# Kernel optimization log

Hardware: AMD Instinct MI355X
Metric: run time of the kernel (lower is better)

The kernel has to match this reference:

```python
import jax, jax.numpy as jnp
import numpy as np

B, N, A, O, D, Q, H = 64, 4, 1024, 128, 256, 256, 128
NEG_INF = -1e30


def setup_inputs() -> dict:
    key = jax.random.key(0)
    ks = jax.random.split(key, 8)
    q = jax.random.normal(ks[0], (B, N, 1, Q), dtype=jnp.float32)
    att1 = jax.random.uniform(ks[1], (B, N, A, O), dtype=jnp.float32)
    obj_reps = jax.random.normal(ks[2], (B, O, D), dtype=jnp.float32)
    tags_attention = jax.random.randint(ks[3], (B, N, A), 0, 2, dtype=jnp.int32)
    W1 = jax.random.normal(ks[4], (D + Q, H), dtype=jnp.float32) / np.sqrt(D + Q)
    b1 = jnp.zeros((H,), dtype=jnp.float32)
    W2 = jax.random.normal(ks[5], (H, 1), dtype=jnp.float32) / np.sqrt(H)
    b2 = jnp.zeros((1,), dtype=jnp.float32)
    return {"q": q, "att1": att1, "obj_reps": obj_reps,
            "tags_attention": tags_attention,
            "W1": W1, "b1": b1, "W2": W2, "b2": b2, "t": 1}


def reference(q, att1, obj_reps, tags_attention, W1, b1, W2, b2, t):
    # v: [B,N,A,D] = att1 [B,N,A,O] @ obj_reps [B,O,D]
    v = jnp.einsum('bnao,bod->bnad', att1, obj_reps)
    # q broadcast over token dim A, concat -> [B,N,A,D+Q]
    q_proj = jnp.broadcast_to(q, v.shape[:3] + (q.shape[-1],))
    vq = jnp.concatenate([v, q_proj], axis=-1)
    # FCNet: Linear + ReLU (dropout is identity at inference)
    joint_repr = jax.nn.relu(vq @ W1 + b1)          # [B,N,A,H]
    logits = (joint_repr @ W2 + b2)[..., 0]          # [B,N,A]
    # temperature-scaled masked softmax over tokens
    masked = jnp.where(tags_attention > 0, logits / t, NEG_INF)
    att2 = jax.nn.softmax(masked, axis=-1)           # [B,N,A]
    # attention_last: [B,N,O] = att2 [B,N,1,A] @ att1 [B,N,A,O]
    return jnp.einsum('bna,bnao->bno', att2, att1)
```

## Files before the change

kernel.cpp:

```cpp
#include <hip/hip_runtime.h>
#include <math.h>

#define Bc 64
#define Nc 4
#define Ac 1024
#define Oc 128
#define Dc 256
#define Qc 256
#define Hc 128
#define BN (Bc*Nc)

using f4     = __attribute__((ext_vector_type(4))) float;
using f32x16 = __attribute__((ext_vector_type(16))) float;
using short8 = __attribute__((ext_vector_type(8))) short;
using us4    = __attribute__((ext_vector_type(4))) unsigned short;

__device__ inline float decode_t(const void* p) {
    int i = *(const int*)p;
    if (i >= 1 && i <= 1000000) return (float)i;
    return __int_as_float(i);
}

__device__ inline unsigned short bf16_rne(float x) {
    unsigned u = __builtin_bit_cast(unsigned, x);
    u += 0x7FFFu + ((u >> 16) & 1u);
    return (unsigned short)(u >> 16);
}

__device__ inline void split_bf16(float x, unsigned short& hi, unsigned short& lo) {
    unsigned u = __builtin_bit_cast(unsigned, x);
    hi = (unsigned short)(u >> 16);
    float hif = __builtin_bit_cast(float, u & 0xFFFF0000u);
    float lof = x - hif;
    lo = (unsigned short)(__builtin_bit_cast(unsigned, lof) >> 16);
}

__global__ __launch_bounds__(256) void prep_M_kernel(
    const float* __restrict__ obj, const float* __restrict__ W1,
    unsigned short* __restrict__ Mt_hi, unsigned short* __restrict__ Mt_lo)
{
    __shared__ float w_s[32][36];
    __shared__ float obj_sT[32][68];

    const int t  = threadIdx.x;
    const int tx = t & 15;
    const int ty = t >> 4;
    const int h0 = blockIdx.x * 32;
    const int o0 = blockIdx.y * 64;
    const int b  = blockIdx.z;
    const int r8 = t >> 3, c8 = t & 7;

    const float* objb = obj + ((size_t)b * Oc + o0) * Dc;

    float acc[2][4];
    #pragma unroll
    for (int i = 0; i < 2; i++)
        #pragma unroll
        for (int j = 0; j < 4; j++) acc[i][j] = 0.f;

    f4 wv  = *(const f4*)(W1 + (size_t)r8 * Hc + h0 + c8 * 4);
    f4 ov0 = *(const f4*)(objb + (size_t)r8 * Dc + c8 * 4);
    f4 ov1 = *(const f4*)(objb + (size_t)(r8 + 32) * Dc + c8 * 4);

    for (int ko = 0; ko < 8; ++ko) {
        *(f4*)&w_s[r8][c8 * 4] = wv;
        obj_sT[c8 * 4 + 0][r8] = ov0[0];
        obj_sT[c8 * 4 + 1][r8] = ov0[1];
        obj_sT[c8 * 4 + 2][r8] = ov0[2];
        obj_sT[c8 * 4 + 3][r8] = ov0[3];
        obj_sT[c8 * 4 + 0][r8 + 32] = ov1[0];
        obj_sT[c8 * 4 + 1][r8 + 32] = ov1[1];
        obj_sT[c8 * 4 + 2][r8 + 32] = ov1[2];
        obj_sT[c8 * 4 + 3][r8 + 32] = ov1[3];
        __syncthreads();
        if (ko < 7) {
            wv  = *(const f4*)(W1 + (size_t)((ko + 1) * 32 + r8) * Hc + h0 + c8 * 4);
            ov0 = *(const f4*)(objb + (size_t)r8 * Dc + (ko + 1) * 32 + c8 * 4);
            ov1 = *(const f4*)(objb + (size_t)(r8 + 32) * Dc + (ko + 1) * 32 + c8 * 4);
        }
        #pragma unroll 4
        for (int k = 0; k < 32; k++) {
            float a0 = w_s[k][ty * 2];
            float a1 = w_s[k][ty * 2 + 1];
            f4 bv = *(const f4*)&obj_sT[k][tx * 4];
            #pragma unroll
            for (int j = 0; j < 4; j++) {
                acc[0][j] += a0 * bv[j];
                acc[1][j] += a1 * bv[j];
            }
        }
        __syncthreads();
    }

    #pragma unroll
    for (int i = 0; i < 2; i++) {
        us4 hi, lo;
        #pragma unroll
        for (int j = 0; j < 4; j++) {
            unsigned short h16, l16;
            split_bf16(acc[i][j], h16, l16);
            hi[j] = h16; lo[j] = l16;
        }
        size_t ofs = ((size_t)b * Hc + h0 + ty * 2 + i) * Oc + o0 + tx * 4;
        *(us4*)(Mt_hi + ofs) = hi;
        *(us4*)(Mt_lo + ofs) = lo;
    }
}

__global__ __launch_bounds__(512) void prep_qb_kernel(
    const float* __restrict__ q, const float* __restrict__ W1,
    const float* __restrict__ b1, float* __restrict__ qb)
{
    __shared__ float qs[256];
    __shared__ float red[4][128];
    const int t = threadIdx.x;
    const int bn = blockIdx.x;

    if (t < 256) qs[t] = q[bn * Qc + t];
    __syncthreads();

    const int h = t & 127, kq = t >> 7;
    float acc = 0.f;
    const float* w = W1 + (size_t)(Dc + kq * 64) * Hc + h;
    #pragma unroll 8
    for (int d = 0; d < 64; ++d)
        acc += qs[kq * 64 + d] * w[(size_t)d * Hc];
    red[kq][h] = acc;
    __syncthreads();

    if (t < 128)
        qb[bn * Hc + t] = b1[t] + red[0][t] + red[1][t] + red[2][t] + red[3][t];
}

__global__ __launch_bounds__(1024, 4) void main_kernel(
    const float* __restrict__ att1, const int* __restrict__ tags,
    const unsigned short* __restrict__ Mt_hi, const unsigned short* __restrict__ Mt_lo,
    const float* __restrict__ qb, const float* __restrict__ W2,
    const float* __restrict__ b2, const void* __restrict__ tptr,
    float* __restrict__ out)
{
    __shared__ unsigned short A_s[2][128][136];
    __shared__ float part2[128][5];
    __shared__ float part3[8][132];
    __shared__ float e_s[128];
    __shared__ float2 qw_s[128];
    __shared__ float zfin[2];

    const int t    = threadIdx.x;
    const int wave = t >> 6;
    const int lane = t & 63;
    const int l31  = lane & 31;
    const int half = lane >> 5;
    const int ag   = wave & 3;
    const int hg   = wave >> 2;
    const int bn = blockIdx.x;
    const int b  = bn >> 2;

    const float* att_bn = att1 + (size_t)bn * Ac * Oc;

    f4 sv[4];
    #pragma unroll
    for (int s = 0; s < 4; s++) {
        int idx = t + 1024 * s;
        sv[s] = *(const f4*)(att_bn + (size_t)idx * 4);
    }

    const size_t arow = ((size_t)b * Hc + hg * 32 + l31) * Oc + half * 8;
    short8 Ah[8], Al[8];
    #pragma unroll
    for (int ks = 0; ks < 8; ks++) {
        Ah[ks] = *(const short8*)(Mt_hi + arow + ks * 16);
        Al[ks] = *(const short8*)(Mt_lo + arow + ks * 16);
    }

    if (t < 128) {
        float2 qw; qw.x = qb[bn * Hc + t]; qw.y = W2[t];
        qw_s[t] = qw;
    }
    int tg_cur = (t < 128) ? tags[(size_t)bn * Ac + t] : 0;
    const float b2v  = b2[0];
    const float tval = decode_t(tptr);

    float z_reg = 0.f, out_reg = 0.f;

    for (int tile = 0; tile < 8; ++tile) {
        const int buf = tile & 1;
        const float* tile_ptr = att_bn + (size_t)tile * 128 * Oc;

        #pragma unroll
        for (int s = 0; s < 4; s++) {
            int idx = t + 1024 * s;
            int r = idx >> 5, c4 = idx & 31;
            us4 h4;
            #pragma unroll
            for (int j = 0; j < 4; j++) h4[j] = bf16_rne(sv[s][j]);
            *(us4*)&A_s[buf][r][c4 * 4] = h4;
        }
        __syncthreads();

        int tg_next = 0;
        if (tile < 7) {
            const float* np = att_bn + (size_t)(tile + 1) * 128 * Oc;
            #pragma unroll
            for (int s = 0; s < 4; s++) {
                int idx = t + 1024 * s;
                sv[s] = *(const f4*)(np + (size_t)idx * 4);
            }
            if (t < 128) tg_next = tags[(size_t)bn * Ac + (tile + 1) * 128 + t];
        }

        f32x16 acc = (f32x16)(0.f);
        #pragma unroll
        for (int ks = 0; ks < 8; ks++) {
            short8 bv = *(const short8*)&A_s[buf][ag * 32 + l31][ks * 16 + half * 8];
            acc = __builtin_amdgcn_mfma_f32_32x32x16_bf16(Ah[ks], bv, acc, 0, 0, 0);
            acc = __builtin_amdgcn_mfma_f32_32x32x16_bf16(Al[ks], bv, acc, 0, 0, 0);
        }

        float p = 0.f;
        #pragma unroll
        for (int reg = 0; reg < 16; reg++) {
            int h = hg * 32 + (reg & 3) + 8 * (reg >> 2) + 4 * half;
            float2 qw = qw_s[h];
            float v = acc[reg] + qw.x;
            v = v > 0.f ? v : 0.f;
            p += v * qw.y;
        }
        p += __shfl_xor(p, 32);
        if (half == 0) part2[ag * 32 + l31][hg] = p;
        __syncthreads();

        if (t < 128) {
            float sum = part2[t][0] + part2[t][1] + part2[t][2] + part2[t][3] + b2v;
            float logit = sum / tval;
            float e = (tg_cur > 0) ? __expf(logit) : 0.f;
            e_s[t] = e;
            z_reg += e;
        }
        __syncthreads();

        {
            const int o = t & 127;
            const int g = t >> 7;
            const float* ab = tile_ptr + (size_t)(g * 16) * Oc + o;
            float accum = 0.f;
            #pragma unroll
            for (int a = 0; a < 16; a++)
                accum += e_s[g * 16 + a] * ab[(size_t)a * Oc];
            part3[g][o] = accum;
        }
        __syncthreads();

        if (t < 128) {
            float s = 0.f;
            #pragma unroll
            for (int g = 0; g < 8; g++) s += part3[g][t];
            out_reg += s;
        }
        tg_cur = tg_next;
    }

    __syncthreads();
    if (t < 128) {
        float z = z_reg;
        #pragma unroll
        for (int off = 32; off > 0; off >>= 1) z += __shfl_down(z, off);
        if (lane == 0) zfin[wave] = z;
    }
    __syncthreads();
    if (t < 128) {
        float Z = zfin[0] + zfin[1];
        out[(size_t)bn * Oc + t] = out_reg / Z;
    }
}

extern "C" void kernel_launch(void* const* d_in, const int* in_sizes, int n_in,
                              void* d_out, int out_size, void* d_ws, size_t ws_size,
                              hipStream_t stream)
{
    (void)in_sizes; (void)n_in; (void)out_size; (void)ws_size;

    const float* q    = (const float*)d_in[0];
    const float* att1 = (const float*)d_in[1];
    const float* obj  = (const float*)d_in[2];
    const int*   tags = (const int*)d_in[3];
    const float* W1   = (const float*)d_in[4];
    const float* b1   = (const float*)d_in[5];
    const float* W2   = (const float*)d_in[6];
    const float* b2   = (const float*)d_in[7];
    const void*  tptr = d_in[8];
    float* out = (float*)d_out;

    char* wsb = (char*)d_ws;
    unsigned short* Mt_hi = (unsigned short*)wsb;
    unsigned short* Mt_lo = (unsigned short*)(wsb + (size_t)2*1024*1024);
    float* qbuf = (float*)(wsb + (size_t)4*1024*1024);

    prep_M_kernel<<<dim3(4, 2, Bc), 256, 0, stream>>>(obj, W1, Mt_hi, Mt_lo);
    prep_qb_kernel<<<dim3(BN), 512, 0, stream>>>(q, W1, b1, qbuf);
    main_kernel<<<dim3(BN), 1024, 0, stream>>>(att1, tags, Mt_hi, Mt_lo,
                                               qbuf, W2, b2, tptr, out);
}
```

Baseline: 252.9 us.

## Split each attention row across two blocks and combine partials in a finalize kernel

```diff
diff --git a/kernel.cpp b/kernel.cpp
--- a/kernel.cpp
+++ b/kernel.cpp
@@ -132,18 +132,18 @@
         qb[bn * Hc + t] = b1[t] + red[0][t] + red[1][t] + red[2][t] + red[3][t];
 }
 
-__global__ __launch_bounds__(1024, 4) void main_kernel(
+__global__ __launch_bounds__(1024, 2) void main_kernel(
     const float* __restrict__ att1, const int* __restrict__ tags,
     const unsigned short* __restrict__ Mt_hi, const unsigned short* __restrict__ Mt_lo,
     const float* __restrict__ qb, const float* __restrict__ W2,
     const float* __restrict__ b2, const void* __restrict__ tptr,
-    float* __restrict__ out)
-{
-    __shared__ unsigned short A_s[2][128][136];
+    float* __restrict__ Zpart, float* __restrict__ outpart)
+{
+    __shared__ unsigned short A_s[128][136];
     __shared__ float part2[128][5];
-    __shared__ float part3[8][132];
     __shared__ float e_s[128];
     __shared__ float2 qw_s[128];
+    __shared__ float out_lds[128];
     __shared__ float zfin[2];
 
     const int t    = threadIdx.x;
@@ -153,16 +153,19 @@
     const int half = lane >> 5;
     const int ag   = wave & 3;
     const int hg   = wave >> 2;
-    const int bn = blockIdx.x;
-    const int b  = bn >> 2;
-
-    const float* att_bn = att1 + (size_t)bn * Ac * Oc;
+    const int bidx = blockIdx.x;
+    const int bn   = bidx >> 1;
+    const int hsel = bidx & 1;
+    const int b    = bn >> 2;
+
+    const float* att_h = att1 + ((size_t)bn * Ac + hsel * 512) * Oc;
+    const int*   tag_h = tags + (size_t)bn * Ac + hsel * 512;
 
     f4 sv[4];
     #pragma unroll
     for (int s = 0; s < 4; s++) {
         int idx = t + 1024 * s;
-        sv[s] = *(const f4*)(att_bn + (size_t)idx * 4);
+        sv[s] = *(const f4*)(att_h + (size_t)idx * 4);
     }
 
     const size_t arow = ((size_t)b * Hc + hg * 32 + l31) * Oc + half * 8;
@@ -176,16 +179,16 @@
     if (t < 128) {
         float2 qw; qw.x = qb[bn * Hc + t]; qw.y = W2[t];
         qw_s[t] = qw;
-    }
-    int tg_cur = (t < 128) ? tags[(size_t)bn * Ac + t] : 0;
+        out_lds[t] = 0.f;
+    }
+    int tg_cur = (t < 128) ? tag_h[t] : 0;
     const float b2v  = b2[0];
     const float tval = decode_t(tptr);
 
-    float z_reg = 0.f, out_reg = 0.f;
-
-    for (int tile = 0; tile < 8; ++tile) {
-        const int buf = tile & 1;
-        const float* tile_ptr = att_bn + (size_t)tile * 128 * Oc;
+    float z_reg = 0.f;
+
+    for (int tile = 0; tile < 4; ++tile) {
+        const float* tile_ptr = att_h + (size_t)tile * 128 * Oc;
 
         #pragma unroll
         for (int s = 0; s < 4; s++) {
@@ -194,25 +197,25 @@
             us4 h4;
             #pragma unroll
             for (int j = 0; j < 4; j++) h4[j] = bf16_rne(sv[s][j]);
-            *(us4*)&A_s[buf][r][c4 * 4] = h4;
+            *(us4*)&A_s[r][c4 * 4] = h4;
         }
         __syncthreads();
 
         int tg_next = 0;
-        if (tile < 7) {
-            const float* np = att_bn + (size_t)(tile + 1) * 128 * Oc;
+        if (tile < 3) {
+            const float* np = att_h + (size_t)(tile + 1) * 128 * Oc;
             #pragma unroll
             for (int s = 0; s < 4; s++) {
                 int idx = t + 1024 * s;
                 sv[s] = *(const f4*)(np + (size_t)idx * 4);
             }
-            if (t < 128) tg_next = tags[(size_t)bn * Ac + (tile + 1) * 128 + t];
+            if (t < 128) tg_next = tag_h[(tile + 1) * 128 + t];
         }
 
         f32x16 acc = (f32x16)(0.f);
         #pragma unroll
         for (int ks = 0; ks < 8; ks++) {
-            short8 bv = *(const short8*)&A_s[buf][ag * 32 + l31][ks * 16 + half * 8];
+            short8 bv = *(const short8*)&A_s[ag * 32 + l31][ks * 16 + half * 8];
             acc = __builtin_amdgcn_mfma_f32_32x32x16_bf16(Ah[ks], bv, acc, 0, 0, 0);
             acc = __builtin_amdgcn_mfma_f32_32x32x16_bf16(Al[ks], bv, acc, 0, 0, 0);
         }
@@ -247,20 +250,13 @@
             #pragma unroll
             for (int a = 0; a < 16; a++)
                 accum += e_s[g * 16 + a] * ab[(size_t)a * Oc];
-            part3[g][o] = accum;
-        }
-        __syncthreads();
-
-        if (t < 128) {
-            float s = 0.f;
-            #pragma unroll
-            for (int g = 0; g < 8; g++) s += part3[g][t];
-            out_reg += s;
-        }
+            atomicAdd(&out_lds[o], accum);
+        }
+        __syncthreads();
+
         tg_cur = tg_next;
     }
 
-    __syncthreads();
     if (t < 128) {
         float z = z_reg;
         #pragma unroll
@@ -268,10 +264,19 @@
         if (lane == 0) zfin[wave] = z;
     }
     __syncthreads();
-    if (t < 128) {
-        float Z = zfin[0] + zfin[1];
-        out[(size_t)bn * Oc + t] = out_reg / Z;
-    }
+    if (t == 0) Zpart[bidx] = zfin[0] + zfin[1];
+    if (t < 128) outpart[(size_t)bidx * 128 + t] = out_lds[t];
+}
+
+__global__ __launch_bounds__(128) void finalize_kernel(
+    const float* __restrict__ Zpart, const float* __restrict__ outpart,
+    float* __restrict__ out)
+{
+    const int bn = blockIdx.x;
+    const int t  = threadIdx.x;
+    float Z = Zpart[2 * bn] + Zpart[2 * bn + 1];
+    float v = outpart[(size_t)(2 * bn) * 128 + t] + outpart[(size_t)(2 * bn + 1) * 128 + t];
+    out[(size_t)bn * Oc + t] = v / Z;
 }
 
 extern "C" void kernel_launch(void* const* d_in, const int* in_sizes, int n_in,
@@ -295,9 +300,12 @@
     unsigned short* Mt_hi = (unsigned short*)wsb;
     unsigned short* Mt_lo = (unsigned short*)(wsb + (size_t)2*1024*1024);
     float* qbuf = (float*)(wsb + (size_t)4*1024*1024);
+    float* Zp   = qbuf + (size_t)BN * Hc;
+    float* opart= Zp + 512;
 
     prep_M_kernel<<<dim3(4, 2, Bc), 256, 0, stream>>>(obj, W1, Mt_hi, Mt_lo);
     prep_qb_kernel<<<dim3(BN), 512, 0, stream>>>(q, W1, b1, qbuf);
-    main_kernel<<<dim3(BN), 1024, 0, stream>>>(att1, tags, Mt_hi, Mt_lo,
-                                               qbuf, W2, b2, tptr, out);
-}
+    main_kernel<<<dim3(2 * BN), 1024, 0, stream>>>(att1, tags, Mt_hi, Mt_lo,
+                                                   qbuf, W2, b2, tptr, Zp, opart);
+    finalize_kernel<<<dim3(BN), 128, 0, stream>>>(Zp, opart, out);
+}
```

Result: slower. 277.8 us (+9.9%).
